# Optimization experiments

Measured on AMD Instinct MI355X. Metric: run time of the kernel, lower is better.

The kernel has to match this reference:

```python
import jax, jax.numpy as jnp
import numpy as np

B, S, V, H, T = 8, 256, 32000, 1024, 4


def setup_inputs() -> dict:
    key = jax.random.key(0)
    ks = jax.random.split(key, 8)
    s_in = 1.0 / np.sqrt(H)
    return {
        "x": jax.random.randint(ks[0], (B, S), 0, V),
        "h_l_init": jnp.zeros((B, H), jnp.float32),
        "h_h_init": jnp.zeros((B, H), jnp.float32),
        "emb": jax.random.normal(ks[1], (V, H), jnp.float32) * 0.02,
        "l_Wih": jax.random.normal(ks[2], (3 * H, 2 * H), jnp.float32) * s_in,
        "l_Whh": jax.random.normal(ks[3], (3 * H, H), jnp.float32) * s_in,
        "l_bih": jnp.zeros((3 * H,), jnp.float32),
        "l_bhh": jnp.zeros((3 * H,), jnp.float32),
        "h_Wih": jax.random.normal(ks[4], (3 * H, H), jnp.float32) * s_in,
        "h_Whh": jax.random.normal(ks[5], (3 * H, H), jnp.float32) * s_in,
        "h_bih": jnp.zeros((3 * H,), jnp.float32),
        "h_bhh": jnp.zeros((3 * H,), jnp.float32),
        "out_W": jax.random.normal(ks[6], (V, H), jnp.float32) * s_in,
        "out_b": jnp.zeros((V,), jnp.float32),
    }


def gru_cell(x, h, Wih, Whh, bih, bhh):
    # PyTorch GRUCell math
    gi = x @ Wih.T + bih  # [B, 3H]
    gh = h @ Whh.T + bhh
    i_r, i_z, i_n = jnp.split(gi, 3, axis=-1)
    h_r, h_z, h_n = jnp.split(gh, 3, axis=-1)
    r = jax.nn.sigmoid(i_r + h_r)
    z = jax.nn.sigmoid(i_z + h_z)
    n = jnp.tanh(i_n + r * h_n)
    return (1.0 - z) * n + z * h


def reference(x, h_l_init, h_h_init, emb, l_Wih, l_Whh, l_bih, l_bhh,
              h_Wih, h_Whh, h_bih, h_bhh, out_W, out_b):
    x_emb = emb[x]  # [B, S, H]
    seq_len = x.shape[1]
    pad_len = (T - seq_len % T) % T
    if pad_len > 0:
        x_emb = jnp.pad(x_emb, ((0, 0), (0, pad_len), (0, 0)))
    total = x_emb.shape[1]
    # [n_blocks, T, B, H]
    xb = x_emb.transpose(1, 0, 2).reshape(total // T, T, x.shape[0], H)

    def block(carry, x_block):
        h_l, h_h = carry

        def step(h_l, x_t):
            h_l = gru_cell(jnp.concatenate([x_t, h_h], axis=-1), h_l,
                           l_Wih, l_Whh, l_bih, l_bhh)
            return h_l, h_l

        h_l, hs = jax.lax.scan(step, h_l, x_block)  # hs: [T, B, H]
        outs = hs @ out_W.T + out_b  # [T, B, V]
        h_h = gru_cell(h_l, h_h, h_Wih, h_Whh, h_bih, h_bhh)
        return (h_l, h_h), outs

    (h_l, h_h), outs = jax.lax.scan(block, (h_l_init, h_h_init), xb)
    # [n_blocks, T, B, V] -> [B, total, V]
    outputs = outs.reshape(total, x.shape[0], -1).transpose(1, 0, 2)
    return outputs[:, :seq_len, :], h_l, h_h
```

## Files before the change

### kernel.cpp

```cpp
#include <hip/hip_runtime.h>
#include <stdint.h>

#define HH    1024
#define H3    3072
#define NB    8
#define SEQ   256
#define MTOK  2048
#define VOCAB 32000

typedef __attribute__((ext_vector_type(8))) short short8;
typedef __attribute__((ext_vector_type(4))) float floatx4;

__device__ __forceinline__ uint16_t f2bf(float f) {
    uint32_t u = __float_as_uint(f);
    return (uint16_t)((u + 0x7FFFu + ((u >> 16) & 1u)) >> 16);
}

__device__ __forceinline__ float sigm(float x) { return 1.0f / (1.0f + __expf(-x)); }

__global__ void kEmbed(const int* __restrict__ x, const float* __restrict__ emb,
                       uint16_t* __restrict__ xe) {
    int m = blockIdx.x;
    int tok = x[m];
    float4 v = *(const float4*)(emb + (size_t)tok * HH + threadIdx.x * 4);
    ushort4 o;
    o.x = f2bf(v.x); o.y = f2bf(v.y); o.z = f2bf(v.z); o.w = f2bf(v.w);
    *(ushort4*)(xe + (size_t)m * HH + threadIdx.x * 4) = o;
}

__global__ __launch_bounds__(256) void kGemm(
    const uint16_t* __restrict__ A, const float* __restrict__ W,
    const float* __restrict__ bias, float* __restrict__ C,
    int N, int strideW) {
    __shared__ uint16_t lA[128 * 64];
    __shared__ uint16_t lB[128 * 64];

    const int tid  = threadIdx.x;
    const int rowT = blockIdx.y * 128;
    const int colT = blockIdx.x * 128;
    const int pos  = tid & 7;
    const int r8   = (tid >> 3) & 7;
    const int ca   = pos ^ r8;
    const int lane = tid & 63, w = tid >> 6;
    const int wm = (w >> 1) * 64, wn = (w & 1) * 64;
    const int l15 = lane & 15, l4 = lane >> 4;

    floatx4 acc[4][4];
    for (int a = 0; a < 4; a++)
        for (int b = 0; b < 4; b++)
            acc[a][b] = (floatx4){0.f, 0.f, 0.f, 0.f};

    for (int it = 0; it < 16; ++it) {
        const int kB = it * 64;
        uint4 av[4]; uint4 bv[4];
        for (int i = 0; i < 4; i++) {
            int row = i * 32 + (tid >> 3);
            av[i] = *(const uint4*)(A + (size_t)(rowT + row) * HH + kB + ca * 8);
            const float* wp = W + (size_t)(colT + row) * strideW + kB + ca * 8;
            float4 w0 = *(const float4*)wp;
            float4 w1 = *(const float4*)(wp + 4);
            uint4 pk;
            pk.x = (uint32_t)f2bf(w0.x) | ((uint32_t)f2bf(w0.y) << 16);
            pk.y = (uint32_t)f2bf(w0.z) | ((uint32_t)f2bf(w0.w) << 16);
            pk.z = (uint32_t)f2bf(w1.x) | ((uint32_t)f2bf(w1.y) << 16);
            pk.w = (uint32_t)f2bf(w1.z) | ((uint32_t)f2bf(w1.w) << 16);
            bv[i] = pk;
        }
        __syncthreads();
        for (int i = 0; i < 4; i++) {
            int slot = i * 256 + tid;
            *(uint4*)(lA + slot * 8) = av[i];
            *(uint4*)(lB + slot * 8) = bv[i];
        }
        __syncthreads();
        for (int ks = 0; ks < 2; ++ks) {
            short8 af[4], bf_[4];
            int kc = ks * 4 + l4;
            for (int mt = 0; mt < 4; mt++) {
                int row = wm + mt * 16 + l15;
                af[mt] = *(const short8*)(lA + row * 64 + ((kc ^ (row & 7)) * 8));
            }
            for (int nt = 0; nt < 4; nt++) {
                int row = wn + nt * 16 + l15;
                bf_[nt] = *(const short8*)(lB + row * 64 + ((kc ^ (row & 7)) * 8));
            }
            for (int mt = 0; mt < 4; mt++)
                for (int nt = 0; nt < 4; nt++)
                    acc[mt][nt] = __builtin_amdgcn_mfma_f32_16x16x32_bf16(
                        af[mt], bf_[nt], acc[mt][nt], 0, 0, 0);
        }
    }
    for (int nt = 0; nt < 4; nt++) {
        int col = colT + wn + nt * 16 + l15;
        float bval = bias[col];
        for (int mt = 0; mt < 4; mt++) {
            int row0 = rowT + wm + mt * 16 + l4 * 4;
            for (int r = 0; r < 4; r++)
                C[(size_t)(row0 + r) * N + col] = acc[mt][nt][r] + bval;
        }
    }
}

__global__ __launch_bounds__(256) void kStep(
    const float* __restrict__ Whh, const float* __restrict__ bhh,
    const float* __restrict__ gix, const float* __restrict__ gih,
    const float* __restrict__ hcur, float* __restrict__ hnxt,
    uint16_t* __restrict__ hs, int s) {
    __shared__ float hsm[NB * HH];
    int tid = threadIdx.x;
    for (int b = 0; b < NB; b++)
        *(float4*)(hsm + b * HH + tid * 4) = *(const float4*)(hcur + b * HH + tid * 4);
    __syncthreads();

    int lane = tid & 63, w = tid >> 6;
    int j = blockIdx.x * 4 + w;
    const float* wr = Whh + (size_t)j * HH;
    const float* wz = Whh + (size_t)(HH + j) * HH;
    const float* wn = Whh + (size_t)(2 * HH + j) * HH;
    float pr[NB], pz[NB], pn[NB];
    for (int b = 0; b < NB; b++) { pr[b] = 0.f; pz[b] = 0.f; pn[b] = 0.f; }
    for (int c = 0; c < 4; c++) {
        int k0 = c * 256 + lane * 4;
        float4 vr = *(const float4*)(wr + k0);
        float4 vz = *(const float4*)(wz + k0);
        float4 vn = *(const float4*)(wn + k0);
        for (int b = 0; b < NB; b++) {
            float4 hv = *(const float4*)(hsm + b * HH + k0);
            pr[b] += vr.x * hv.x + vr.y * hv.y + vr.z * hv.z + vr.w * hv.w;
            pz[b] += vz.x * hv.x + vz.y * hv.y + vz.z * hv.z + vz.w * hv.w;
            pn[b] += vn.x * hv.x + vn.y * hv.y + vn.z * hv.z + vn.w * hv.w;
        }
    }
    for (int off = 1; off < 64; off <<= 1)
        for (int b = 0; b < NB; b++) {
            pr[b] += __shfl_xor(pr[b], off, 64);
            pz[b] += __shfl_xor(pz[b], off, 64);
            pn[b] += __shfl_xor(pn[b], off, 64);
        }
    if (lane < NB) {
        int b = lane;
        size_t m = (size_t)b * SEQ + s;
        float ir = gix[m * H3 + j]          + gih[b * H3 + j];
        float iz = gix[m * H3 + HH + j]     + gih[b * H3 + HH + j];
        float in_ = gix[m * H3 + 2 * HH + j] + gih[b * H3 + 2 * HH + j];
        float hr = pr[b] + bhh[j];
        float hz = pz[b] + bhh[HH + j];
        float hn = pn[b] + bhh[2 * HH + j];
        float r = sigm(ir + hr);
        float z = sigm(iz + hz);
        float n = tanhf(in_ + r * hn);
        float hnew = (1.f - z) * n + z * hsm[b * HH + j];
        hnxt[b * HH + j] = hnew;
        hs[m * HH + j] = f2bf(hnew);
    }
}

__global__ __launch_bounds__(256) void kHGRU(
    const float* __restrict__ Wih, const float* __restrict__ Whh,
    const float* __restrict__ bih, const float* __restrict__ bhh,
    const float* __restrict__ xl, const float* __restrict__ hcur,
    float* __restrict__ hnxt) {
    __shared__ float sx[NB * HH];
    __shared__ float sh[NB * HH];
    int tid = threadIdx.x;
    for (int b = 0; b < NB; b++) {
        *(float4*)(sx + b * HH + tid * 4) = *(const float4*)(xl + b * HH + tid * 4);
        *(float4*)(sh + b * HH + tid * 4) = *(const float4*)(hcur + b * HH + tid * 4);
    }
    __syncthreads();
    int lane = tid & 63, w = tid >> 6;
    int j = blockIdx.x * 4 + w;
    const float* wir = Wih + (size_t)j * HH;
    const float* wiz = Wih + (size_t)(HH + j) * HH;
    const float* win = Wih + (size_t)(2 * HH + j) * HH;
    const float* whr = Whh + (size_t)j * HH;
    const float* whz = Whh + (size_t)(HH + j) * HH;
    const float* whn = Whh + (size_t)(2 * HH + j) * HH;
    float air[NB], aiz[NB], ain[NB], ahr[NB], ahz[NB], ahn[NB];
    for (int b = 0; b < NB; b++) { air[b]=aiz[b]=ain[b]=ahr[b]=ahz[b]=ahn[b]=0.f; }
    for (int c = 0; c < 4; c++) {
        int k0 = c * 256 + lane * 4;
        float4 vir = *(const float4*)(wir + k0);
        float4 viz = *(const float4*)(wiz + k0);
        float4 vin = *(const float4*)(win + k0);
        float4 vhr = *(const float4*)(whr + k0);
        float4 vhz = *(const float4*)(whz + k0);
        float4 vhn = *(const float4*)(whn + k0);
        for (int b = 0; b < NB; b++) {
            float4 xv = *(const float4*)(sx + b * HH + k0);
            float4 hv = *(const float4*)(sh + b * HH + k0);
            air[b] += vir.x*xv.x + vir.y*xv.y + vir.z*xv.z + vir.w*xv.w;
            aiz[b] += viz.x*xv.x + viz.y*xv.y + viz.z*xv.z + viz.w*xv.w;
            ain[b] += vin.x*xv.x + vin.y*xv.y + vin.z*xv.z + vin.w*xv.w;
            ahr[b] += vhr.x*hv.x + vhr.y*hv.y + vhr.z*hv.z + vhr.w*hv.w;
            ahz[b] += vhz.x*hv.x + vhz.y*hv.y + vhz.z*hv.z + vhz.w*hv.w;
            ahn[b] += vhn.x*hv.x + vhn.y*hv.y + vhn.z*hv.z + vhn.w*hv.w;
        }
    }
    for (int off = 1; off < 64; off <<= 1)
        for (int b = 0; b < NB; b++) {
            air[b] += __shfl_xor(air[b], off, 64);
            aiz[b] += __shfl_xor(aiz[b], off, 64);
            ain[b] += __shfl_xor(ain[b], off, 64);
            ahr[b] += __shfl_xor(ahr[b], off, 64);
            ahz[b] += __shfl_xor(ahz[b], off, 64);
            ahn[b] += __shfl_xor(ahn[b], off, 64);
        }
    if (lane < NB) {
        int b = lane;
        float ir = air[b] + bih[j],      hr = ahr[b] + bhh[j];
        float iz = aiz[b] + bih[HH + j], hz = ahz[b] + bhh[HH + j];
        float in_ = ain[b] + bih[2*HH+j], hn = ahn[b] + bhh[2*HH+j];
        float r = sigm(ir + hr);
        float z = sigm(iz + hz);
        float n = tanhf(in_ + r * hn);
        hnxt[b * HH + j] = (1.f - z) * n + z * sh[b * HH + j];
    }
}

__global__ __launch_bounds__(256) void kGih(
    const float* __restrict__ Wcol, const float* __restrict__ hh,
    float* __restrict__ gih) {
    __shared__ float sh[NB * HH];
    int tid = threadIdx.x;
    for (int b = 0; b < NB; b++)
        *(float4*)(sh + b * HH + tid * 4) = *(const float4*)(hh + b * HH + tid * 4);
    __syncthreads();
    int lane = tid & 63, w = tid >> 6;
    int nbase = blockIdx.x * 12 + w * 3;
    const float* w0 = Wcol + (size_t)(nbase + 0) * 2048;
    const float* w1 = Wcol + (size_t)(nbase + 1) * 2048;
    const float* w2 = Wcol + (size_t)(nbase + 2) * 2048;
    float a0[NB], a1[NB], a2[NB];
    for (int b = 0; b < NB; b++) { a0[b] = a1[b] = a2[b] = 0.f; }
    for (int c = 0; c < 4; c++) {
        int k0 = c * 256 + lane * 4;
        float4 v0 = *(const float4*)(w0 + k0);
        float4 v1 = *(const float4*)(w1 + k0);
        float4 v2 = *(const float4*)(w2 + k0);
        for (int b = 0; b < NB; b++) {
            float4 hv = *(const float4*)(sh + b * HH + k0);
            a0[b] += v0.x*hv.x + v0.y*hv.y + v0.z*hv.z + v0.w*hv.w;
            a1[b] += v1.x*hv.x + v1.y*hv.y + v1.z*hv.z + v1.w*hv.w;
            a2[b] += v2.x*hv.x + v2.y*hv.y + v2.z*hv.z + v2.w*hv.w;
        }
    }
    for (int off = 1; off < 64; off <<= 1)
        for (int b = 0; b < NB; b++) {
            a0[b] += __shfl_xor(a0[b], off, 64);
            a1[b] += __shfl_xor(a1[b], off, 64);
            a2[b] += __shfl_xor(a2[b], off, 64);
        }
    if (lane < NB) {
        int b = lane;
        gih[b * H3 + nbase + 0] = a0[b];
        gih[b * H3 + nbase + 1] = a1[b];
        gih[b * H3 + nbase + 2] = a2[b];
    }
}

__global__ void kTail(const float* __restrict__ hl, const float* __restrict__ hh,
                      float* __restrict__ dst) {
    int i = blockIdx.x * 256 + threadIdx.x;
    if (i < NB * HH) dst[i] = hl[i];
    else if (i < 2 * NB * HH) dst[i] = hh[i - NB * HH];
}

extern "C" void kernel_launch(void* const* d_in, const int* in_sizes, int n_in,
                              void* d_out, int out_size, void* d_ws, size_t ws_size,
                              hipStream_t stream) {
    const int*   x    = (const int*)  d_in[0];
    const float* hl0  = (const float*)d_in[1];
    const float* hh0  = (const float*)d_in[2];
    const float* emb  = (const float*)d_in[3];
    const float* lWih = (const float*)d_in[4];
    const float* lWhh = (const float*)d_in[5];
    const float* lbih = (const float*)d_in[6];
    const float* lbhh = (const float*)d_in[7];
    const float* hWih = (const float*)d_in[8];
    const float* hWhh = (const float*)d_in[9];
    const float* hbih = (const float*)d_in[10];
    const float* hbhh = (const float*)d_in[11];
    const float* outW = (const float*)d_in[12];
    const float* outb = (const float*)d_in[13];
    float* out = (float*)d_out;

    char* p = (char*)d_ws;
    float* gix = (float*)p;        p += (size_t)MTOK * H3 * 4;
    float* gih = (float*)p;        p += (size_t)NB * H3 * 4;
    float* hbufL = (float*)p;      p += 2 * (size_t)NB * HH * 4;
    float* hbufH = (float*)p;      p += 2 * (size_t)NB * HH * 4;
    uint16_t* hs = (uint16_t*)p;   p += (size_t)MTOK * HH * 2;
    uint16_t* xe = (uint16_t*)p;   p += (size_t)MTOK * HH * 2;

    hipMemcpyAsync(hbufL, hl0, (size_t)NB * HH * 4, hipMemcpyDeviceToDevice, stream);
    hipMemcpyAsync(hbufH, hh0, (size_t)NB * HH * 4, hipMemcpyDeviceToDevice, stream);

    kEmbed<<<MTOK, 256, 0, stream>>>(x, emb, xe);
    kGemm<<<dim3(H3 / 128, MTOK / 128), 256, 0, stream>>>(xe, lWih, lbih, gix, H3, 2048);
    kGih<<<256, 256, 0, stream>>>(lWih + HH, hbufH, gih);

    for (int blk = 0; blk < 64; ++blk) {
        for (int t = 0; t < 4; ++t) {
            int g = blk * 4 + t;
            const float* hc = hbufL + (g & 1) * NB * HH;
            float* hn = hbufL + ((g + 1) & 1) * NB * HH;
            kStep<<<256, 256, 0, stream>>>(lWhh, lbhh, gix, gih, hc, hn, hs, g);
        }
        const float* hhc = hbufH + (blk & 1) * NB * HH;
        float* hhn = hbufH + ((blk + 1) & 1) * NB * HH;
        kHGRU<<<256, 256, 0, stream>>>(hWih, hWhh, hbih, hbhh, hbufL, hhc, hhn);
        if (blk < 63)
            kGih<<<256, 256, 0, stream>>>(lWih + HH, hhn, gih);
    }

    kGemm<<<dim3(VOCAB / 128, MTOK / 128), 256, 0, stream>>>(hs, outW, outb, out, VOCAB, 1024);
    kTail<<<64, 256, 0, stream>>>(hbufL, hbufH, out + (size_t)MTOK * VOCAB);
}
```

Baseline: 3.671 ms.

## Fuse recurrent scan into persistent kernel with grid barriers; pre-convert weights to bf16

Replaces the roughly 450 per-step kernel launches (kStep, kHGRU, kGih) with one persistent kScan kernel of 256 workgroups that synchronises through an atomic grid barrier. Each wave keeps its rows of the low-level Whh in registers across steps, and the h-GRU and context-projection work is folded into the same loop. Reductions use a scatter-reduce shuffle pattern instead of full butterflies per batch element. The GEMM weights are also converted to bf16 in separate passes, which removes the in-loop fp32 to bf16 conversion but adds extra kernels. The grid barrier relies on all 256 workgroups being resident at the same time, otherwise it can deadlock.

Result: slower. 14.67 ms (+299.6%).

```diff
diff --git a/kernel.cpp b/kernel.cpp
--- a/kernel.cpp
+++ b/kernel.cpp
@@ -7,6 +7,7 @@
 #define SEQ   256
 #define MTOK  2048
 #define VOCAB 32000
+#define NWG   256
 
 typedef __attribute__((ext_vector_type(8))) short short8;
 typedef __attribute__((ext_vector_type(4))) float floatx4;
@@ -28,10 +29,18 @@
     *(ushort4*)(xe + (size_t)m * HH + threadIdx.x * 4) = o;
 }
 
+__global__ void kConv(const float* __restrict__ src, uint16_t* __restrict__ dst,
+                      int stride) {
+    int row = blockIdx.x;
+    float4 v = *(const float4*)(src + (size_t)row * stride + threadIdx.x * 4);
+    ushort4 o;
+    o.x = f2bf(v.x); o.y = f2bf(v.y); o.z = f2bf(v.z); o.w = f2bf(v.w);
+    *(ushort4*)(dst + (size_t)row * HH + threadIdx.x * 4) = o;
+}
+
 __global__ __launch_bounds__(256) void kGemm(
-    const uint16_t* __restrict__ A, const float* __restrict__ W,
-    const float* __restrict__ bias, float* __restrict__ C,
-    int N, int strideW) {
+    const uint16_t* __restrict__ A, const uint16_t* __restrict__ W,
+    const float* __restrict__ bias, float* __restrict__ C, int N) {
     __shared__ uint16_t lA[128 * 64];
     __shared__ uint16_t lB[128 * 64];
 
@@ -50,6 +59,68 @@
         for (int b = 0; b < 4; b++)
             acc[a][b] = (floatx4){0.f, 0.f, 0.f, 0.f};
 
+    for (int it = 0; it < 16; ++it) {
+        const int kB = it * 64;
+        uint4 av[4]; uint4 bv[4];
+        for (int i = 0; i < 4; i++) {
+            int row = i * 32 + (tid >> 3);
+            av[i] = *(const uint4*)(A + (size_t)(rowT + row) * HH + kB + ca * 8);
+            bv[i] = *(const uint4*)(W + (size_t)(colT + row) * HH + kB + ca * 8);
+        }
+        __syncthreads();
+        for (int i = 0; i < 4; i++) {
+            int slot = i * 256 + tid;
+            *(uint4*)(lA + slot * 8) = av[i];
+            *(uint4*)(lB + slot * 8) = bv[i];
+        }
+        __syncthreads();
+        for (int ks = 0; ks < 2; ++ks) {
+            short8 af[4], bf_[4];
+            int kc = ks * 4 + l4;
+            for (int mt = 0; mt < 4; mt++) {
+                int row = wm + mt * 16 + l15;
+                af[mt] = *(const short8*)(lA + row * 64 + ((kc ^ (row & 7)) * 8));
+            }
+            for (int nt = 0; nt < 4; nt++) {
+                int row = wn + nt * 16 + l15;
+                bf_[nt] = *(const short8*)(lB + row * 64 + ((kc ^ (row & 7)) * 8));
+            }
+            for (int mt = 0; mt < 4; mt++)
+                for (int nt = 0; nt < 4; nt++)
+                    acc[mt][nt] = __builtin_amdgcn_mfma_f32_16x16x32_bf16(
+                        af[mt], bf_[nt], acc[mt][nt], 0, 0, 0);
+        }
+    }
+    for (int nt = 0; nt < 4; nt++) {
+        int col = colT + wn + nt * 16 + l15;
+        float bval = bias[col];
+        for (int mt = 0; mt < 4; mt++) {
+            int row0 = rowT + wm + mt * 16 + l4 * 4;
+            for (int r = 0; r < 4; r++)
+                C[(size_t)(row0 + r) * N + col] = acc[mt][nt][r] + bval;
+        }
+    }
+}
+
+__global__ __launch_bounds__(256) void kGemmF(
+    const uint16_t* __restrict__ A, const float* __restrict__ W,
+    const float* __restrict__ bias, float* __restrict__ C,
+    int N, int strideW) {
+    __shared__ uint16_t lA[128 * 64];
+    __shared__ uint16_t lB[128 * 64];
+    const int tid  = threadIdx.x;
+    const int rowT = blockIdx.y * 128;
+    const int colT = blockIdx.x * 128;
+    const int pos  = tid & 7;
+    const int r8   = (tid >> 3) & 7;
+    const int ca   = pos ^ r8;
+    const int lane = tid & 63, w = tid >> 6;
+    const int wm = (w >> 1) * 64, wn = (w & 1) * 64;
+    const int l15 = lane & 15, l4 = lane >> 4;
+    floatx4 acc[4][4];
+    for (int a = 0; a < 4; a++)
+        for (int b = 0; b < 4; b++)
+            acc[a][b] = (floatx4){0.f, 0.f, 0.f, 0.f};
     for (int it = 0; it < 16; ++it) {
         const int kB = it * 64;
         uint4 av[4]; uint4 bv[4];
@@ -101,161 +172,223 @@
     }
 }
 
-__global__ __launch_bounds__(256) void kStep(
-    const float* __restrict__ Whh, const float* __restrict__ bhh,
-    const float* __restrict__ gix, const float* __restrict__ gih,
-    const float* __restrict__ hcur, float* __restrict__ hnxt,
-    uint16_t* __restrict__ hs, int s) {
+__device__ __forceinline__ float redScatter(float (&p)[NB], int lane) {
+    float q[4];
+#pragma unroll
+    for (int i = 0; i < 4; i++) {
+        float kk = (lane & 1) ? p[4 + i] : p[i];
+        float ss = (lane & 1) ? p[i] : p[4 + i];
+        q[i] = kk + __shfl_xor(ss, 1, 64);
+    }
+    float r[2];
+#pragma unroll
+    for (int i = 0; i < 2; i++) {
+        float kk = (lane & 2) ? q[2 + i] : q[i];
+        float ss = (lane & 2) ? q[i] : q[2 + i];
+        r[i] = kk + __shfl_xor(ss, 2, 64);
+    }
+    float kk = (lane & 4) ? r[1] : r[0];
+    float ss = (lane & 4) ? r[0] : r[1];
+    float v = kk + __shfl_xor(ss, 4, 64);
+    v += __shfl_xor(v, 8, 64);
+    v += __shfl_xor(v, 16, 64);
+    v += __shfl_xor(v, 32, 64);
+    return v;
+}
+
+__device__ __forceinline__ void gbar(unsigned* cnt, unsigned* gen) {
+    __syncthreads();
+    if (threadIdx.x == 0) {
+        unsigned g = __hip_atomic_load(gen, __ATOMIC_RELAXED, __HIP_MEMORY_SCOPE_AGENT);
+        unsigned a = __hip_atomic_fetch_add(cnt, 1u, __ATOMIC_ACQ_REL, __HIP_MEMORY_SCOPE_AGENT);
+        if (a == NWG - 1u) {
+            __hip_atomic_store(cnt, 0u, __ATOMIC_RELAXED, __HIP_MEMORY_SCOPE_AGENT);
+            __hip_atomic_store(gen, g + 1u, __ATOMIC_RELEASE, __HIP_MEMORY_SCOPE_AGENT);
+        } else {
+            while (__hip_atomic_load(gen, __ATOMIC_RELAXED, __HIP_MEMORY_SCOPE_AGENT) == g)
+                __builtin_amdgcn_s_sleep(1);
+        }
+    }
+    __syncthreads();
+    __builtin_amdgcn_fence(__ATOMIC_ACQUIRE, "agent");
+}
+
+__global__ __launch_bounds__(256, 2) void kScan(
+    const float* __restrict__ lWih,
+    const float* __restrict__ lWhh,
+    const float* __restrict__ lbhh,
+    const float* __restrict__ hWih, const float* __restrict__ hWhh,
+    const float* __restrict__ hbih, const float* __restrict__ hbhh,
+    const float* __restrict__ gix,
+    float* __restrict__ hL,
+    float* __restrict__ hH,
+    uint16_t* __restrict__ hs,
+    unsigned* __restrict__ syncb)
+{
     __shared__ float hsm[NB * HH];
-    int tid = threadIdx.x;
-    for (int b = 0; b < NB; b++)
-        *(float4*)(hsm + b * HH + tid * 4) = *(const float4*)(hcur + b * HH + tid * 4);
-    __syncthreads();
-
-    int lane = tid & 63, w = tid >> 6;
-    int j = blockIdx.x * 4 + w;
-    const float* wr = Whh + (size_t)j * HH;
-    const float* wz = Whh + (size_t)(HH + j) * HH;
-    const float* wn = Whh + (size_t)(2 * HH + j) * HH;
-    float pr[NB], pz[NB], pn[NB];
-    for (int b = 0; b < NB; b++) { pr[b] = 0.f; pz[b] = 0.f; pn[b] = 0.f; }
+    __shared__ float hhm[NB * HH];
+
+    unsigned* cnt = syncb;
+    unsigned* gen = syncb + 1;
+    const int tid  = threadIdx.x;
+    const int lane = tid & 63, wv = tid >> 6;
+    const int j    = blockIdx.x * 4 + wv;
+    const int beta = ((lane & 1) << 2) | (lane & 2) | ((lane >> 2) & 1);
+
+    const float br  = lbhh[j], bz = lbhh[HH + j], bn = lbhh[2 * HH + j];
+    const float hbr = hbih[j], hbz = hbih[HH + j], hbn = hbih[2 * HH + j];
+    const float ghr = hbhh[j], ghz = hbhh[HH + j], ghn = hbhh[2 * HH + j];
+
+    const float* wr_l = lWhh + (size_t)j * HH;
+    const float* wz_l = lWhh + (size_t)(HH + j) * HH;
+    const float* wn_l = lWhh + (size_t)(2 * HH + j) * HH;
+    float4 wvr[4], wvz[4], wvn[4];
+#pragma unroll
     for (int c = 0; c < 4; c++) {
         int k0 = c * 256 + lane * 4;
-        float4 vr = *(const float4*)(wr + k0);
-        float4 vz = *(const float4*)(wz + k0);
-        float4 vn = *(const float4*)(wn + k0);
-        for (int b = 0; b < NB; b++) {
-            float4 hv = *(const float4*)(hsm + b * HH + k0);
-            pr[b] += vr.x * hv.x + vr.y * hv.y + vr.z * hv.z + vr.w * hv.w;
-            pz[b] += vz.x * hv.x + vz.y * hv.y + vz.z * hv.z + vz.w * hv.w;
-            pn[b] += vn.x * hv.x + vn.y * hv.y + vn.z * hv.z + vn.w * hv.w;
-        }
-    }
-    for (int off = 1; off < 64; off <<= 1)
-        for (int b = 0; b < NB; b++) {
-            pr[b] += __shfl_xor(pr[b], off, 64);
-            pz[b] += __shfl_xor(pz[b], off, 64);
-            pn[b] += __shfl_xor(pn[b], off, 64);
-        }
-    if (lane < NB) {
-        int b = lane;
-        size_t m = (size_t)b * SEQ + s;
-        float ir = gix[m * H3 + j]          + gih[b * H3 + j];
-        float iz = gix[m * H3 + HH + j]     + gih[b * H3 + HH + j];
-        float in_ = gix[m * H3 + 2 * HH + j] + gih[b * H3 + 2 * HH + j];
-        float hr = pr[b] + bhh[j];
-        float hz = pz[b] + bhh[HH + j];
-        float hn = pn[b] + bhh[2 * HH + j];
-        float r = sigm(ir + hr);
-        float z = sigm(iz + hz);
-        float n = tanhf(in_ + r * hn);
-        float hnew = (1.f - z) * n + z * hsm[b * HH + j];
-        hnxt[b * HH + j] = hnew;
-        hs[m * HH + j] = f2bf(hnew);
-    }
-}
-
-__global__ __launch_bounds__(256) void kHGRU(
-    const float* __restrict__ Wih, const float* __restrict__ Whh,
-    const float* __restrict__ bih, const float* __restrict__ bhh,
-    const float* __restrict__ xl, const float* __restrict__ hcur,
-    float* __restrict__ hnxt) {
-    __shared__ float sx[NB * HH];
-    __shared__ float sh[NB * HH];
-    int tid = threadIdx.x;
-    for (int b = 0; b < NB; b++) {
-        *(float4*)(sx + b * HH + tid * 4) = *(const float4*)(xl + b * HH + tid * 4);
-        *(float4*)(sh + b * HH + tid * 4) = *(const float4*)(hcur + b * HH + tid * 4);
-    }
-    __syncthreads();
-    int lane = tid & 63, w = tid >> 6;
-    int j = blockIdx.x * 4 + w;
-    const float* wir = Wih + (size_t)j * HH;
-    const float* wiz = Wih + (size_t)(HH + j) * HH;
-    const float* win = Wih + (size_t)(2 * HH + j) * HH;
-    const float* whr = Whh + (size_t)j * HH;
-    const float* whz = Whh + (size_t)(HH + j) * HH;
-    const float* whn = Whh + (size_t)(2 * HH + j) * HH;
-    float air[NB], aiz[NB], ain[NB], ahr[NB], ahz[NB], ahn[NB];
-    for (int b = 0; b < NB; b++) { air[b]=aiz[b]=ain[b]=ahr[b]=ahz[b]=ahn[b]=0.f; }
-    for (int c = 0; c < 4; c++) {
-        int k0 = c * 256 + lane * 4;
-        float4 vir = *(const float4*)(wir + k0);
-        float4 viz = *(const float4*)(wiz + k0);
-        float4 vin = *(const float4*)(win + k0);
-        float4 vhr = *(const float4*)(whr + k0);
-        float4 vhz = *(const float4*)(whz + k0);
-        float4 vhn = *(const float4*)(whn + k0);
-        for (int b = 0; b < NB; b++) {
-            float4 xv = *(const float4*)(sx + b * HH + k0);
-            float4 hv = *(const float4*)(sh + b * HH + k0);
-            air[b] += vir.x*xv.x + vir.y*xv.y + vir.z*xv.z + vir.w*xv.w;
-            aiz[b] += viz.x*xv.x + viz.y*xv.y + viz.z*xv.z + viz.w*xv.w;
-            ain[b] += vin.x*xv.x + vin.y*xv.y + vin.z*xv.z + vin.w*xv.w;
-            ahr[b] += vhr.x*hv.x + vhr.y*hv.y + vhr.z*hv.z + vhr.w*hv.w;
-            ahz[b] += vhz.x*hv.x + vhz.y*hv.y + vhz.z*hv.z + vhz.w*hv.w;
-            ahn[b] += vhn.x*hv.x + vhn.y*hv.y + vhn.z*hv.z + vhn.w*hv.w;
-        }
-    }
-    for (int off = 1; off < 64; off <<= 1)
-        for (int b = 0; b < NB; b++) {
-            air[b] += __shfl_xor(air[b], off, 64);
-            aiz[b] += __shfl_xor(aiz[b], off, 64);
-            ain[b] += __shfl_xor(ain[b], off, 64);
-            ahr[b] += __shfl_xor(ahr[b], off, 64);
-            ahz[b] += __shfl_xor(ahz[b], off, 64);
-            ahn[b] += __shfl_xor(ahn[b], off, 64);
-        }
-    if (lane < NB) {
-        int b = lane;
-        float ir = air[b] + bih[j],      hr = ahr[b] + bhh[j];
-        float iz = aiz[b] + bih[HH + j], hz = ahz[b] + bhh[HH + j];
-        float in_ = ain[b] + bih[2*HH+j], hn = ahn[b] + bhh[2*HH+j];
-        float r = sigm(ir + hr);
-        float z = sigm(iz + hz);
-        float n = tanhf(in_ + r * hn);
-        hnxt[b * HH + j] = (1.f - z) * n + z * sh[b * HH + j];
-    }
-}
-
-__global__ __launch_bounds__(256) void kGih(
-    const float* __restrict__ Wcol, const float* __restrict__ hh,
-    float* __restrict__ gih) {
-    __shared__ float sh[NB * HH];
-    int tid = threadIdx.x;
-    for (int b = 0; b < NB; b++)
-        *(float4*)(sh + b * HH + tid * 4) = *(const float4*)(hh + b * HH + tid * 4);
-    __syncthreads();
-    int lane = tid & 63, w = tid >> 6;
-    int nbase = blockIdx.x * 12 + w * 3;
-    const float* w0 = Wcol + (size_t)(nbase + 0) * 2048;
-    const float* w1 = Wcol + (size_t)(nbase + 1) * 2048;
-    const float* w2 = Wcol + (size_t)(nbase + 2) * 2048;
-    float a0[NB], a1[NB], a2[NB];
-    for (int b = 0; b < NB; b++) { a0[b] = a1[b] = a2[b] = 0.f; }
-    for (int c = 0; c < 4; c++) {
-        int k0 = c * 256 + lane * 4;
-        float4 v0 = *(const float4*)(w0 + k0);
-        float4 v1 = *(const float4*)(w1 + k0);
-        float4 v2 = *(const float4*)(w2 + k0);
-        for (int b = 0; b < NB; b++) {
-            float4 hv = *(const float4*)(sh + b * HH + k0);
-            a0[b] += v0.x*hv.x + v0.y*hv.y + v0.z*hv.z + v0.w*hv.w;
-            a1[b] += v1.x*hv.x + v1.y*hv.y + v1.z*hv.z + v1.w*hv.w;
-            a2[b] += v2.x*hv.x + v2.y*hv.y + v2.z*hv.z + v2.w*hv.w;
-        }
-    }
-    for (int off = 1; off < 64; off <<= 1)
-        for (int b = 0; b < NB; b++) {
-            a0[b] += __shfl_xor(a0[b], off, 64);
-            a1[b] += __shfl_xor(a1[b], off, 64);
-            a2[b] += __shfl_xor(a2[b], off, 64);
-        }
-    if (lane < NB) {
-        int b = lane;
-        gih[b * H3 + nbase + 0] = a0[b];
-        gih[b * H3 + nbase + 1] = a1[b];
-        gih[b * H3 + nbase + 2] = a2[b];
+        wvr[c] = *(const float4*)(wr_l + k0);
+        wvz[c] = *(const float4*)(wz_l + k0);
+        wvn[c] = *(const float4*)(wn_l + k0);
+    }
+    const float* wr_c = lWih + (size_t)j * 2048 + HH;
+    const float* wz_c = lWih + (size_t)(HH + j) * 2048 + HH;
+    const float* wn_c = lWih + (size_t)(2 * HH + j) * 2048 + HH;
+
+    float gr = 0.f, gz = 0.f, gn = 0.f;
+
+    for (int s = 0; s < SEQ; ++s) {
+        const int t = s & 3, blk = s >> 2;
+        const float* hcur = hL + (s & 1) * (NB * HH);
+        float* hnxt = hL + ((s + 1) & 1) * (NB * HH);
+
+        const size_t m = (size_t)beta * SEQ + s;
+        const float gxr = gix[m * H3 + j];
+        const float gxz = gix[m * H3 + HH + j];
+        const float gxn = gix[m * H3 + 2 * HH + j];
+
+        if (s == 0 || t != 0) {
+#pragma unroll
+            for (int i = 0; i < 8; i++)
+                ((float4*)hsm)[i * 256 + tid] = ((const float4*)hcur)[i * 256 + tid];
+        }
+        if (t == 0) {
+            const float* hhc = hH + (blk & 1) * (NB * HH);
+#pragma unroll
+            for (int i = 0; i < 8; i++)
+                ((float4*)hhm)[i * 256 + tid] = ((const float4*)hhc)[i * 256 + tid];
+        }
+        __syncthreads();
+
+        if (t == 0) {
+            float ar[NB], az[NB], an[NB];
+#pragma unroll
+            for (int b = 0; b < NB; b++) { ar[b] = 0.f; az[b] = 0.f; an[b] = 0.f; }
+#pragma unroll
+            for (int c = 0; c < 4; c++) {
+                int k0 = c * 256 + lane * 4;
+                float4 vr = *(const float4*)(wr_c + k0);
+                float4 vz = *(const float4*)(wz_c + k0);
+                float4 vn = *(const float4*)(wn_c + k0);
+#pragma unroll
+                for (int b = 0; b < NB; b++) {
+                    float4 hv = *(const float4*)(hhm + b * HH + k0);
+                    ar[b] += vr.x * hv.x + vr.y * hv.y + vr.z * hv.z + vr.w * hv.w;
+                    az[b] += vz.x * hv.x + vz.y * hv.y + vz.z * hv.z + vz.w * hv.w;
+                    an[b] += vn.x * hv.x + vn.y * hv.y + vn.z * hv.z + vn.w * hv.w;
+                }
+            }
+            gr = redScatter(ar, lane);
+            gz = redScatter(az, lane);
+            gn = redScatter(an, lane);
+        }
+
+        float pr[NB], pz[NB], pn[NB];
+#pragma unroll
+        for (int b = 0; b < NB; b++) { pr[b] = 0.f; pz[b] = 0.f; pn[b] = 0.f; }
+#pragma unroll
+        for (int c = 0; c < 4; c++) {
+            int k0 = c * 256 + lane * 4;
+            float4 vr = wvr[c], vz = wvz[c], vn = wvn[c];
+#pragma unroll
+            for (int b = 0; b < NB; b++) {
+                float4 hv = *(const float4*)(hsm + b * HH + k0);
+                pr[b] += vr.x * hv.x + vr.y * hv.y + vr.z * hv.z + vr.w * hv.w;
+                pz[b] += vz.x * hv.x + vz.y * hv.y + vz.z * hv.z + vz.w * hv.w;
+                pn[b] += vn.x * hv.x + vn.y * hv.y + vn.z * hv.z + vn.w * hv.w;
+            }
+        }
+        float sr = redScatter(pr, lane);
+        float sz = redScatter(pz, lane);
+        float sn = redScatter(pn, lane);
+
+        if (lane < NB) {
+            float hr = sr + br, hz = sz + bz, hn = sn + bn;
+            float r  = sigm(gxr + gr + hr);
+            float z  = sigm(gxz + gz + hz);
+            float n  = tanhf(gxn + gn + r * hn);
+            float hold = hsm[beta * HH + j];
+            float hnew = (1.f - z) * n + z * hold;
+            hnxt[beta * HH + j] = hnew;
+            hs[m * HH + j] = f2bf(hnew);
+        }
+        gbar(cnt, gen);
+
+        if (t == 3) {
+            const float* hhc = hH + (blk & 1) * (NB * HH);
+            float* hhn = hH + ((blk + 1) & 1) * (NB * HH);
+            (void)hhc;
+#pragma unroll
+            for (int i = 0; i < 8; i++)
+                ((float4*)hsm)[i * 256 + tid] = ((const float4*)hL)[i * 256 + tid];
+            __syncthreads();
+            const float* wir = hWih + (size_t)j * HH;
+            const float* wiz = hWih + (size_t)(HH + j) * HH;
+            const float* win = hWih + (size_t)(2 * HH + j) * HH;
+            const float* whr = hWhh + (size_t)j * HH;
+            const float* whz = hWhh + (size_t)(HH + j) * HH;
+            const float* whn = hWhh + (size_t)(2 * HH + j) * HH;
+            float air[NB], aiz[NB], ain[NB], ahr[NB], ahz[NB], ahn[NB];
+#pragma unroll
+            for (int b = 0; b < NB; b++) {
+                air[b] = 0.f; aiz[b] = 0.f; ain[b] = 0.f;
+                ahr[b] = 0.f; ahz[b] = 0.f; ahn[b] = 0.f;
+            }
+#pragma unroll
+            for (int c = 0; c < 4; c++) {
+                int k0 = c * 256 + lane * 4;
+                float4 vir = *(const float4*)(wir + k0);
+                float4 viz = *(const float4*)(wiz + k0);
+                float4 vin = *(const float4*)(win + k0);
+                float4 vhr = *(const float4*)(whr + k0);
+                float4 vhz = *(const float4*)(whz + k0);
+                float4 vhn = *(const float4*)(whn + k0);
+#pragma unroll
+                for (int b = 0; b < NB; b++) {
+                    float4 xv = *(const float4*)(hsm + b * HH + k0);
+                    float4 hv = *(const float4*)(hhm + b * HH + k0);
+                    air[b] += vir.x * xv.x + vir.y * xv.y + vir.z * xv.z + vir.w * xv.w;
+                    aiz[b] += viz.x * xv.x + viz.y * xv.y + viz.z * xv.z + viz.w * xv.w;
+                    ain[b] += vin.x * xv.x + vin.y * xv.y + vin.z * xv.z + vin.w * xv.w;
+                    ahr[b] += vhr.x * hv.x + vhr.y * hv.y + vhr.z * hv.z + vhr.w * hv.w;
+                    ahz[b] += vhz.x * hv.x + vhz.y * hv.y + vhz.z * hv.z + vhz.w * hv.w;
+                    ahn[b] += vhn.x * hv.x + vhn.y * hv.y + vhn.z * hv.z + vhn.w * hv.w;
+                }
+            }
+            float sir  = redScatter(air, lane) + hbr;
+            float siz  = redScatter(aiz, lane) + hbz;
+            float sin_ = redScatter(ain, lane) + hbn;
+            float shr  = redScatter(ahr, lane) + ghr;
+            float shz  = redScatter(ahz, lane) + ghz;
+            float shn  = redScatter(ahn, lane) + ghn;
+            if (lane < NB) {
+                float r = sigm(sir + shr);
+                float z = sigm(siz + shz);
+                float n = tanhf(sin_ + r * shn);
+                float hnew = (1.f - z) * n + z * hhm[beta * HH + j];
+                hhn[beta * HH + j] = hnew;
+            }
+            gbar(cnt, gen);
+        }
     }
 }
 
@@ -286,34 +419,36 @@
     float* out = (float*)d_out;
 
     char* p = (char*)d_ws;
-    float* gix = (float*)p;        p += (size_t)MTOK * H3 * 4;
-    float* gih = (float*)p;        p += (size_t)NB * H3 * 4;
-    float* hbufL = (float*)p;      p += 2 * (size_t)NB * HH * 4;
-    float* hbufH = (float*)p;      p += 2 * (size_t)NB * HH * 4;
-    uint16_t* hs = (uint16_t*)p;   p += (size_t)MTOK * HH * 2;
-    uint16_t* xe = (uint16_t*)p;   p += (size_t)MTOK * HH * 2;
+    float* gix = (float*)p;          p += (size_t)MTOK * H3 * 4;
+    float* hbufL = (float*)p;        p += 2 * (size_t)NB * HH * 4;
+    float* hbufH = (float*)p;        p += 2 * (size_t)NB * HH * 4;
+    unsigned* syncb = (unsigned*)p;  p += 256;
+    uint16_t* hsb = (uint16_t*)p;    p += (size_t)MTOK * HH * 2;
+    uint16_t* xe = (uint16_t*)p;     p += (size_t)MTOK * HH * 2;
+    uint16_t* lWihB = (uint16_t*)p;  p += (size_t)H3 * HH * 2;
+    uint16_t* outWB = (uint16_t*)p;  p += (size_t)VOCAB * HH * 2;
+    const bool bf16w = (size_t)(p - (char*)d_ws) <= ws_size;
 
     hipMemcpyAsync(hbufL, hl0, (size_t)NB * HH * 4, hipMemcpyDeviceToDevice, stream);
     hipMemcpyAsync(hbufH, hh0, (size_t)NB * HH * 4, hipMemcpyDeviceToDevice, stream);
+    hipMemsetAsync(syncb, 0, 256, stream);
 
     kEmbed<<<MTOK, 256, 0, stream>>>(x, emb, xe);
-    kGemm<<<dim3(H3 / 128, MTOK / 128), 256, 0, stream>>>(xe, lWih, lbih, gix, H3, 2048);
-    kGih<<<256, 256, 0, stream>>>(lWih + HH, hbufH, gih);
-
-    for (int blk = 0; blk < 64; ++blk) {
-        for (int t = 0; t < 4; ++t) {
-            int g = blk * 4 + t;
-            const float* hc = hbufL + (g & 1) * NB * HH;
-            float* hn = hbufL + ((g + 1) & 1) * NB * HH;
-            kStep<<<256, 256, 0, stream>>>(lWhh, lbhh, gix, gih, hc, hn, hs, g);
-        }
-        const float* hhc = hbufH + (blk & 1) * NB * HH;
-        float* hhn = hbufH + ((blk + 1) & 1) * NB * HH;
-        kHGRU<<<256, 256, 0, stream>>>(hWih, hWhh, hbih, hbhh, hbufL, hhc, hhn);
-        if (blk < 63)
-            kGih<<<256, 256, 0, stream>>>(lWih + HH, hhn, gih);
-    }
-
-    kGemm<<<dim3(VOCAB / 128, MTOK / 128), 256, 0, stream>>>(hs, outW, outb, out, VOCAB, 1024);
+    if (bf16w) {
+        kConv<<<H3, 256, 0, stream>>>(lWih, lWihB, 2048);
+        kGemm<<<dim3(H3 / 128, MTOK / 128), 256, 0, stream>>>(xe, lWihB, lbih, gix, H3);
+    } else {
+        kGemmF<<<dim3(H3 / 128, MTOK / 128), 256, 0, stream>>>(xe, lWih, lbih, gix, H3, 2048);
+    }
+
+    kScan<<<NWG, 256, 0, stream>>>(lWih, lWhh, lbhh, hWih, hWhh, hbih, hbhh,
+                                   gix, hbufL, hbufH, hsb, syncb);
+
+    if (bf16w) {
+        kConv<<<VOCAB, 256, 0, stream>>>(outW, outWB, 1024);
+        kGemm<<<dim3(VOCAB / 128, MTOK / 128), 256, 0, stream>>>(hsb, outWB, outb, out, VOCAB);
+    } else {
+        kGemmF<<<dim3(VOCAB / 128, MTOK / 128), 256, 0, stream>>>(hsb, outW, outb, out, VOCAB, 1024);
+    }
     kTail<<<64, 256, 0, stream>>>(hbufL, hbufH, out + (size_t)MTOK * VOCAB);
 }
```
